# Optimization experiments

Measured on AMD Instinct MI355X. Metric: run time of the kernel, lower is better.

Reference implementation:

```python
import jax, jax.numpy as jnp
import numpy as np

NORM_EPS = 1e-8   # eps in F.normalize
PDIST_EPS = 1e-6  # eps in nn.PairwiseDistance(2, eps=1e-06): ||x1 - x2 + eps||_2


def setup_inputs() -> dict:
    key = jax.random.key(0)
    student_output = jax.random.normal(key, (16384, 1024), dtype=jnp.float32)
    return {"student_output": student_output}


def reference(student_output) -> jnp.ndarray:
    x = student_output
    n = x.shape[0]
    # --- pairwise NN via inner products on L2-normalized vectors (no-grad in original) ---
    norms = jnp.linalg.norm(x, axis=-1, keepdims=True)
    xn = x / jnp.maximum(norms, NORM_EPS)          # F.normalize(x, p=2, eps=1e-8)
    dots = xn @ xn.T                               # [N, N]
    dots = dots.at[jnp.diag_indices(n)].set(-1.0)  # mask self-similarity
    I = jnp.argmax(dots, axis=1)                   # nearest neighbor indices
    # --- pairwise L2 distance to NN (torch adds eps to the difference) ---
    diff = x - x[I] + PDIST_EPS                    # [N, D]
    distances = jnp.sqrt(jnp.sum(diff * diff, axis=-1))
    loss = -jnp.mean(jnp.log(distances))
    return loss
```

## Files before the change

### kernel.cpp

```cpp
#include <hip/hip_runtime.h>
#include <hip/hip_bf16.h>

#define KN 16384
#define KD 1024
#define NB (KN / 128)

typedef __attribute__((ext_vector_type(4))) int   i32x4;
typedef __attribute__((ext_vector_type(8))) int   i32x8;
typedef __attribute__((ext_vector_type(4))) float f32x4;

#define SCALE_M6 0x79797979
#define FMT_FP4  4

__device__ __forceinline__ i32x8 ldg_frag4(const unsigned char* p) {
  const i32x4 v = *(const i32x4*)p;
  return __builtin_shufflevector(v, v, 0, 1, 2, 3, -1, -1, -1, -1);
}

#define IDX_MASK 0x3FFFu
#define VAL_MASK 0xFFFFC000u

__device__ __forceinline__ unsigned fp4n(float x) {
  const float a = fabsf(x);
  unsigned c = (unsigned)(a >= 0.25f) + (unsigned)(a >= 0.75f)
             + (unsigned)(a >= 1.25f) + (unsigned)(a >= 1.75f)
             + (unsigned)(a >= 2.5f)  + (unsigned)(a >= 3.5f)
             + (unsigned)(a >= 5.0f);
  return c | ((__float_as_uint(x) >> 28) & 8u);
}
__device__ __forceinline__ unsigned short pack4(float4 v, float s) {
  return (unsigned short)(fp4n(v.x * s)        | (fp4n(v.y * s) << 4) |
                          (fp4n(v.z * s) << 8) | (fp4n(v.w * s) << 12));
}

__global__ __launch_bounds__(256) void k_normalize(const float* __restrict__ x,
                                                   unsigned char* __restrict__ xn,
                                                   unsigned* __restrict__ best) {
  const int lane = threadIdx.x & 63;
  const int wave = threadIdx.x >> 6;
  const int row  = (blockIdx.x << 2) + wave;
  if (lane == 0) best[row] = 0u;
  const float4* xr = (const float4*)(x + (size_t)row * KD);
  const float4 v0 = xr[lane];
  const float4 v1 = xr[lane + 64];
  const float4 v2 = xr[lane + 128];
  const float4 v3 = xr[lane + 192];
  float ss = v0.x * v0.x + v0.y * v0.y + v0.z * v0.z + v0.w * v0.w
           + v1.x * v1.x + v1.y * v1.y + v1.z * v1.z + v1.w * v1.w
           + v2.x * v2.x + v2.y * v2.y + v2.z * v2.z + v2.w * v2.w
           + v3.x * v3.x + v3.y * v3.y + v3.z * v3.z + v3.w * v3.w;
#pragma unroll
  for (int off = 32; off > 0; off >>= 1) ss += __shfl_xor(ss, off);
  const float scale = 64.0f / fmaxf(sqrtf(ss), 1e-8f);
  const unsigned short s0 = pack4(v0, scale);
  const unsigned short s1 = pack4(v1, scale);
  const unsigned short s2 = pack4(v2, scale);
  const unsigned short s3 = pack4(v3, scale);
  unsigned char* base = xn + ((size_t)(row >> 4) << 13) + (((lane >> 3) & 3) << 8)
                      + ((row & 15) << 4) + ((lane & 7) << 1) + ((lane >> 5) << 10);
  *(unsigned short*)(base)        = s0;
  *(unsigned short*)(base + 2048) = s1;
  *(unsigned short*)(base + 4096) = s2;
  *(unsigned short*)(base + 6144) = s3;
}

template <bool DIAG>
__device__ __forceinline__ void epilogue(const f32x4 (&acc)[4][4], int by, int bx,
                                         int wm, int wn, int quad, int l15,
                                         unsigned* __restrict__ best) {
  const int rowbase = (by << 7) + wm * 64 + (quad << 2);
  const int colbase = (bx << 7) + wn * 64 + l15;
  unsigned cm0 = 0u, cm1 = 0u, cm2 = 0u, cm3 = 0u;
#pragma unroll
  for (int i = 0; i < 4; i++) {
#pragma unroll
    for (int r = 0; r < 4; r++) {
      const int grow = rowbase + i * 16 + r;
      const unsigned grx = (unsigned)grow ^ IDX_MASK;
      unsigned rm = 0u;
#pragma unroll
      for (int j = 0; j < 4; j++) {
        const int gcol = colbase + j * 16;
        unsigned t = (__float_as_uint(fmaf(acc[i][j][r], 0.125f, 3.0f)) << 9) & VAL_MASK;
        if (DIAG && gcol == grow) t = 0u;
        const unsigned rc = t | ((unsigned)gcol ^ IDX_MASK);
        const unsigned cc = t | grx;
        rm = rm > rc ? rm : rc;
        if (j == 0) cm0 = cm0 > cc ? cm0 : cc;
        if (j == 1) cm1 = cm1 > cc ? cm1 : cc;
        if (j == 2) cm2 = cm2 > cc ? cm2 : cc;
        if (j == 3) cm3 = cm3 > cc ? cm3 : cc;
      }
#pragma unroll
      for (int off = 1; off < 16; off <<= 1) {
        const unsigned o = __shfl_xor(rm, off);
        rm = rm > o ? rm : o;
      }
      if (l15 == 0) atomicMax(best + grow, rm);
    }
  }
  if (!DIAG) {
    unsigned cm[4] = {cm0, cm1, cm2, cm3};
#pragma unroll
    for (int j = 0; j < 4; j++) {
      unsigned o = __shfl_xor(cm[j], 16);
      cm[j] = cm[j] > o ? cm[j] : o;
      o = __shfl_xor(cm[j], 32);
      cm[j] = cm[j] > o ? cm[j] : o;
      if (quad == 0) atomicMax(best + colbase + j * 16, cm[j]);
    }
  }
}

__global__ __launch_bounds__(256, 4) void k_nn_argmax(const unsigned char* __restrict__ xn,
                                                      unsigned* __restrict__ best) {
  const int id = blockIdx.x;
  int d, by;
  if (id < 8192) {
    const int o   = id & 7;
    const int idp = id >> 3;
    const int k   = idp >> 6;
    const int p   = idp & 63;
    const int q   = o + (k << 3);
    by = ((q & 15) << 3) + (p & 7);
    d  = ((q >> 4) << 3) + (p >> 3);
  } else {
    d  = NB / 2;
    by = id - 8192;
  }
  const int bx = (by + d) & (NB - 1);

  const int tid  = threadIdx.x;
  const int lane = tid & 63;
  const int wave = tid >> 6;
  const int wm   = wave >> 1;
  const int wn   = wave & 1;
  const int quad = lane >> 4;
  const int l15  = lane & 15;

  f32x4 acc[4][4];
#pragma unroll
  for (int i = 0; i < 4; i++)
#pragma unroll
    for (int j = 0; j < 4; j++) acc[i][j] = (f32x4){0.f, 0.f, 0.f, 0.f};

  const unsigned char* pa = xn + ((size_t)((by << 3) + (wm << 2)) << 13) + (lane << 4);
  const unsigned char* pb = xn + ((size_t)((bx << 3) + (wn << 2)) << 13) + (lane << 4);

#pragma unroll 2
  for (int kb = 0; kb < 8; kb++) {
    const int ko = kb << 10;
    const i32x8 a0 = ldg_frag4(pa + ko);
    const i32x8 a1 = ldg_frag4(pa + (1 << 13) + ko);
    const i32x8 a2 = ldg_frag4(pa + (2 << 13) + ko);
    const i32x8 a3 = ldg_frag4(pa + (3 << 13) + ko);
    const i32x8 b0 = ldg_frag4(pb + ko);
    const i32x8 b1 = ldg_frag4(pb + (1 << 13) + ko);
    const i32x8 b2 = ldg_frag4(pb + (2 << 13) + ko);
    const i32x8 b3 = ldg_frag4(pb + (3 << 13) + ko);
    acc[0][0] = __builtin_amdgcn_mfma_scale_f32_16x16x128_f8f6f4(a0, b0, acc[0][0], FMT_FP4, FMT_FP4, 0, SCALE_M6, 0, SCALE_M6);
    acc[1][0] = __builtin_amdgcn_mfma_scale_f32_16x16x128_f8f6f4(a1, b0, acc[1][0], FMT_FP4, FMT_FP4, 0, SCALE_M6, 0, SCALE_M6);
    acc[2][0] = __builtin_amdgcn_mfma_scale_f32_16x16x128_f8f6f4(a2, b0, acc[2][0], FMT_FP4, FMT_FP4, 0, SCALE_M6, 0, SCALE_M6);
    acc[3][0] = __builtin_amdgcn_mfma_scale_f32_16x16x128_f8f6f4(a3, b0, acc[3][0], FMT_FP4, FMT_FP4, 0, SCALE_M6, 0, SCALE_M6);
    acc[0][1] = __builtin_amdgcn_mfma_scale_f32_16x16x128_f8f6f4(a0, b1, acc[0][1], FMT_FP4, FMT_FP4, 0, SCALE_M6, 0, SCALE_M6);
    acc[1][1] = __builtin_amdgcn_mfma_scale_f32_16x16x128_f8f6f4(a1, b1, acc[1][1], FMT_FP4, FMT_FP4, 0, SCALE_M6, 0, SCALE_M6);
    acc[2][1] = __builtin_amdgcn_mfma_scale_f32_16x16x128_f8f6f4(a2, b1, acc[2][1], FMT_FP4, FMT_FP4, 0, SCALE_M6, 0, SCALE_M6);
    acc[3][1] = __builtin_amdgcn_mfma_scale_f32_16x16x128_f8f6f4(a3, b1, acc[3][1], FMT_FP4, FMT_FP4, 0, SCALE_M6, 0, SCALE_M6);
    acc[0][2] = __builtin_amdgcn_mfma_scale_f32_16x16x128_f8f6f4(a0, b2, acc[0][2], FMT_FP4, FMT_FP4, 0, SCALE_M6, 0, SCALE_M6);
    acc[1][2] = __builtin_amdgcn_mfma_scale_f32_16x16x128_f8f6f4(a1, b2, acc[1][2], FMT_FP4, FMT_FP4, 0, SCALE_M6, 0, SCALE_M6);
    acc[2][2] = __builtin_amdgcn_mfma_scale_f32_16x16x128_f8f6f4(a2, b2, acc[2][2], FMT_FP4, FMT_FP4, 0, SCALE_M6, 0, SCALE_M6);
    acc[3][2] = __builtin_amdgcn_mfma_scale_f32_16x16x128_f8f6f4(a3, b2, acc[3][2], FMT_FP4, FMT_FP4, 0, SCALE_M6, 0, SCALE_M6);
    acc[0][3] = __builtin_amdgcn_mfma_scale_f32_16x16x128_f8f6f4(a0, b3, acc[0][3], FMT_FP4, FMT_FP4, 0, SCALE_M6, 0, SCALE_M6);
    acc[1][3] = __builtin_amdgcn_mfma_scale_f32_16x16x128_f8f6f4(a1, b3, acc[1][3], FMT_FP4, FMT_FP4, 0, SCALE_M6, 0, SCALE_M6);
    acc[2][3] = __builtin_amdgcn_mfma_scale_f32_16x16x128_f8f6f4(a2, b3, acc[2][3], FMT_FP4, FMT_FP4, 0, SCALE_M6, 0, SCALE_M6);
    acc[3][3] = __builtin_amdgcn_mfma_scale_f32_16x16x128_f8f6f4(a3, b3, acc[3][3], FMT_FP4, FMT_FP4, 0, SCALE_M6, 0, SCALE_M6);
  }

  if (d == 0) epilogue<true>(acc, by, bx, wm, wn, quad, l15, best);
  else        epilogue<false>(acc, by, bx, wm, wn, quad, l15, best);
}

__global__ __launch_bounds__(256) void k_dist(const float* __restrict__ x,
                                              const unsigned* __restrict__ best,
                                              float* __restrict__ rowlog) {
  const int lane = threadIdx.x & 63;
  const int wave = threadIdx.x >> 6;
  const int row  = (blockIdx.x << 2) + wave;
  const int nb   = (int)((~best[row]) & IDX_MASK);
  const float4* ar = (const float4*)(x + (size_t)row * KD);
  const float4* br = (const float4*)(x + (size_t)nb * KD);
  float ss = 0.f;
#pragma unroll
  for (int q = 0; q < 4; q++) {
    const float4 a = ar[lane + 64 * q];
    const float4 b = br[lane + 64 * q];
    const float dx = a.x - b.x + 1e-6f;
    const float dy = a.y - b.y + 1e-6f;
    const float dz = a.z - b.z + 1e-6f;
    const float dw = a.w - b.w + 1e-6f;
    ss += dx * dx + dy * dy + dz * dz + dw * dw;
  }
#pragma unroll
  for (int off = 32; off > 0; off >>= 1) ss += __shfl_xor(ss, off);
  if (lane == 0) rowlog[row] = -logf(sqrtf(ss));
}

__global__ __launch_bounds__(1024) void k_final(const float* __restrict__ rowlog,
                                                float* __restrict__ out) {
  const int tid = threadIdx.x;
  float s = 0.f;
  for (int i = tid; i < KN; i += 1024) s += rowlog[i];
#pragma unroll
  for (int off = 32; off > 0; off >>= 1) s += __shfl_down(s, off);
  __shared__ float ws[16];
  if ((tid & 63) == 0) ws[tid >> 6] = s;
  __syncthreads();
  if (tid == 0) {
    float t = 0.f;
#pragma unroll
    for (int i = 0; i < 16; i++) t += ws[i];
    out[0] = t / (float)KN;
  }
}

extern "C" void kernel_launch(void* const* d_in, const int* in_sizes, int n_in,
                              void* d_out, int out_size, void* d_ws, size_t ws_size,
                              hipStream_t stream) {
  const float* x = (const float*)d_in[0];
  float* out = (float*)d_out;

  char* ws = (char*)d_ws;
  unsigned char* xn = (unsigned char*)ws;
  unsigned* best = (unsigned*)(ws + (size_t)KN * KD / 2);
  float* rowlog = (float*)(ws + (size_t)KN * KD / 2 + (size_t)KN * 4);

  k_normalize<<<KN / 4, 256, 0, stream>>>(x, xn, best);
  k_nn_argmax<<<8192 + 64, 256, 0, stream>>>(xn, best);
  k_dist<<<KN / 4, 256, 0, stream>>>(x, best, rowlog);
  k_final<<<1, 1024, 0, stream>>>(rowlog, out);
}
```

Baseline: 241.9 us.

## Stage FP4 tiles through double-buffered LDS with global_load_lds

Each wave used to load its A and B fragments straight from global memory, so every row chunk was fetched by two waves of the block. Now the four waves cooperatively copy the block's A and B K-slices into a double-buffered 32 KB shared-memory tile with direct global-to-LDS loads. The MFMA fragments are then read from LDS, and the next slice is prefetched while the current one is computed. This halves global/L2 fetches per block, but it adds a barrier per K step and LDS usage, and the min-blocks launch bound is relaxed, which may reduce occupancy.

```diff
diff --git a/kernel.cpp b/kernel.cpp
--- a/kernel.cpp
+++ b/kernel.cpp
@@ -9,10 +9,13 @@
 typedef __attribute__((ext_vector_type(8))) int   i32x8;
 typedef __attribute__((ext_vector_type(4))) float f32x4;
 
+typedef __attribute__((address_space(1))) unsigned int gu32;
+typedef __attribute__((address_space(3))) unsigned int su32;
+
 #define SCALE_M6 0x79797979
 #define FMT_FP4  4
 
-__device__ __forceinline__ i32x8 ldg_frag4(const unsigned char* p) {
+__device__ __forceinline__ i32x8 frag4(const unsigned char* p) {
   const i32x4 v = *(const i32x4*)p;
   return __builtin_shufflevector(v, v, 0, 1, 2, 3, -1, -1, -1, -1);
 }
@@ -112,8 +115,10 @@
   }
 }
 
-__global__ __launch_bounds__(256, 4) void k_nn_argmax(const unsigned char* __restrict__ xn,
-                                                      unsigned* __restrict__ best) {
+__global__ __launch_bounds__(256) void k_nn_argmax(const unsigned char* __restrict__ xn,
+                                                   unsigned* __restrict__ best) {
+  __shared__ unsigned char smem[2][16384];
+
   const int id = blockIdx.x;
   int d, by;
   if (id < 8192) {
@@ -144,20 +149,39 @@
 #pragma unroll
     for (int j = 0; j < 4; j++) acc[i][j] = (f32x4){0.f, 0.f, 0.f, 0.f};
 
-  const unsigned char* pa = xn + ((size_t)((by << 3) + (wm << 2)) << 13) + (lane << 4);
-  const unsigned char* pb = xn + ((size_t)((bx << 3) + (wn << 2)) << 13) + (lane << 4);
-
-#pragma unroll 2
+  const int c0 = wave << 2;
+  const int g0 = (wave & 2) ? ((bx << 3) + (c0 & 7)) : ((by << 3) + c0);
+  const unsigned char* sbase = xn + ((size_t)g0 << 13) + (lane << 4);
+
+  const int aoff = (wm << 12) + (lane << 4);
+  const int boff = 8192 + (wn << 12) + (lane << 4);
+
+#pragma unroll
+  for (int t = 0; t < 4; t++)
+    __builtin_amdgcn_global_load_lds((const gu32*)(const void*)(sbase + ((size_t)t << 13)),
+                                     (su32*)(void*)(&smem[0][(c0 + t) << 10]), 16, 0, 0);
+
+#pragma unroll
   for (int kb = 0; kb < 8; kb++) {
-    const int ko = kb << 10;
-    const i32x8 a0 = ldg_frag4(pa + ko);
-    const i32x8 a1 = ldg_frag4(pa + (1 << 13) + ko);
-    const i32x8 a2 = ldg_frag4(pa + (2 << 13) + ko);
-    const i32x8 a3 = ldg_frag4(pa + (3 << 13) + ko);
-    const i32x8 b0 = ldg_frag4(pb + ko);
-    const i32x8 b1 = ldg_frag4(pb + (1 << 13) + ko);
-    const i32x8 b2 = ldg_frag4(pb + (2 << 13) + ko);
-    const i32x8 b3 = ldg_frag4(pb + (3 << 13) + ko);
+    const int buf = kb & 1;
+    __syncthreads();
+    if (kb < 7) {
+#pragma unroll
+      for (int t = 0; t < 4; t++)
+        __builtin_amdgcn_global_load_lds(
+            (const gu32*)(const void*)(sbase + ((size_t)t << 13) + ((size_t)(kb + 1) << 10)),
+            (su32*)(void*)(&smem[buf ^ 1][(c0 + t) << 10]), 16, 0, 0);
+    }
+    const unsigned char* A = &smem[buf][aoff];
+    const unsigned char* B = &smem[buf][boff];
+    const i32x8 a0 = frag4(A);
+    const i32x8 a1 = frag4(A + 1024);
+    const i32x8 a2 = frag4(A + 2048);
+    const i32x8 a3 = frag4(A + 3072);
+    const i32x8 b0 = frag4(B);
+    const i32x8 b1 = frag4(B + 1024);
+    const i32x8 b2 = frag4(B + 2048);
+    const i32x8 b3 = frag4(B + 3072);
     acc[0][0] = __builtin_amdgcn_mfma_scale_f32_16x16x128_f8f6f4(a0, b0, acc[0][0], FMT_FP4, FMT_FP4, 0, SCALE_M6, 0, SCALE_M6);
     acc[1][0] = __builtin_amdgcn_mfma_scale_f32_16x16x128_f8f6f4(a1, b0, acc[1][0], FMT_FP4, FMT_FP4, 0, SCALE_M6, 0, SCALE_M6);
     acc[2][0] = __builtin_amdgcn_mfma_scale_f32_16x16x128_f8f6f4(a2, b0, acc[2][0], FMT_FP4, FMT_FP4, 0, SCALE_M6, 0, SCALE_M6);
```

After: 250.3 us. 1.03x slower.

## Stage A row panel in LDS and reuse it across eight diagonal tiles

Applied to the files above, without the earlier changes.

The argmax GEMM kernel now launches one block per row-block and diagonal group instead of one block per tile. Each block copies its 64KB FP4 A panel into shared memory with global_load_lds, then loops over 8 column tiles. Inside that loop, A fragments are read from LDS and only B still comes from global memory. This halves global/L2 fragment traffic and cuts block launch count. In exchange, 64KB of LDS per block limits occupancy, the 4-block launch bound is dropped, the panel load has no overlap with compute, and the d=64 tail now runs 128 blocks that compute mirrored duplicate tiles.

```diff
diff --git a/kernel.cpp b/kernel.cpp
--- a/kernel.cpp
+++ b/kernel.cpp
@@ -9,10 +9,13 @@
 typedef __attribute__((ext_vector_type(8))) int   i32x8;
 typedef __attribute__((ext_vector_type(4))) float f32x4;
 
+typedef __attribute__((address_space(1))) unsigned int gu32;
+typedef __attribute__((address_space(3))) unsigned int su32;
+
 #define SCALE_M6 0x79797979
 #define FMT_FP4  4
 
-__device__ __forceinline__ i32x8 ldg_frag4(const unsigned char* p) {
+__device__ __forceinline__ i32x8 frag4(const unsigned char* p) {
   const i32x4 v = *(const i32x4*)p;
   return __builtin_shufflevector(v, v, 0, 1, 2, 3, -1, -1, -1, -1);
 }
@@ -112,23 +115,14 @@
   }
 }
 
-__global__ __launch_bounds__(256, 4) void k_nn_argmax(const unsigned char* __restrict__ xn,
-                                                      unsigned* __restrict__ best) {
+__global__ __launch_bounds__(256) void k_nn_argmax(const unsigned char* __restrict__ xn,
+                                                   unsigned* __restrict__ best) {
+  __shared__ unsigned char As[65536];
+
   const int id = blockIdx.x;
-  int d, by;
-  if (id < 8192) {
-    const int o   = id & 7;
-    const int idp = id >> 3;
-    const int k   = idp >> 6;
-    const int p   = idp & 63;
-    const int q   = o + (k << 3);
-    by = ((q & 15) << 3) + (p & 7);
-    d  = ((q >> 4) << 3) + (p >> 3);
-  } else {
-    d  = NB / 2;
-    by = id - 8192;
-  }
-  const int bx = (by + d) & (NB - 1);
+  int by, d0, ntiles;
+  if (id < 1024) { by = id & 127; d0 = (id >> 7) << 3; ntiles = 8; }
+  else           { by = id - 1024; d0 = 64;            ntiles = 1; }
 
   const int tid  = threadIdx.x;
   const int lane = tid & 63;
@@ -138,46 +132,60 @@
   const int quad = lane >> 4;
   const int l15  = lane & 15;
 
-  f32x4 acc[4][4];
-#pragma unroll
-  for (int i = 0; i < 4; i++)
-#pragma unroll
-    for (int j = 0; j < 4; j++) acc[i][j] = (f32x4){0.f, 0.f, 0.f, 0.f};
-
-  const unsigned char* pa = xn + ((size_t)((by << 3) + (wm << 2)) << 13) + (lane << 4);
-  const unsigned char* pb = xn + ((size_t)((bx << 3) + (wn << 2)) << 13) + (lane << 4);
+  const unsigned char* srcA = xn + ((size_t)(by << 6) << 10) + (lane << 4);
+#pragma unroll
+  for (int t = 0; t < 16; t++) {
+    const int c = (wave << 4) + t;
+    __builtin_amdgcn_global_load_lds((const gu32*)(const void*)(srcA + ((size_t)c << 10)),
+                                     (su32*)(void*)(&As[c << 10]), 16, 0, 0);
+  }
+  __syncthreads();
+
+  const int aoff = (wm << 15) + (lane << 4);
+
+  for (int t = 0; t < ntiles; t++) {
+    const int d  = d0 + t;
+    const int bx = (by + d) & (NB - 1);
+    const unsigned char* pb = xn + ((size_t)((bx << 3) + (wn << 2)) << 13) + (lane << 4);
+
+    f32x4 acc[4][4];
+#pragma unroll
+    for (int i = 0; i < 4; i++)
+#pragma unroll
+      for (int j = 0; j < 4; j++) acc[i][j] = (f32x4){0.f, 0.f, 0.f, 0.f};
 
 #pragma unroll 2
-  for (int kb = 0; kb < 8; kb++) {
-    const int ko = kb << 10;
-    const i32x8 a0 = ldg_frag4(pa + ko);
-    const i32x8 a1 = ldg_frag4(pa + (1 << 13) + ko);
-    const i32x8 a2 = ldg_frag4(pa + (2 << 13) + ko);
-    const i32x8 a3 = ldg_frag4(pa + (3 << 13) + ko);
-    const i32x8 b0 = ldg_frag4(pb + ko);
-    const i32x8 b1 = ldg_frag4(pb + (1 << 13) + ko);
-    const i32x8 b2 = ldg_frag4(pb + (2 << 13) + ko);
-    const i32x8 b3 = ldg_frag4(pb + (3 << 13) + ko);
-    acc[0][0] = __builtin_amdgcn_mfma_scale_f32_16x16x128_f8f6f4(a0, b0, acc[0][0], FMT_FP4, FMT_FP4, 0, SCALE_M6, 0, SCALE_M6);
-    acc[1][0] = __builtin_amdgcn_mfma_scale_f32_16x16x128_f8f6f4(a1, b0, acc[1][0], FMT_FP4, FMT_FP4, 0, SCALE_M6, 0, SCALE_M6);
-    acc[2][0] = __builtin_amdgcn_mfma_scale_f32_16x16x128_f8f6f4(a2, b0, acc[2][0], FMT_FP4, FMT_FP4, 0, SCALE_M6, 0, SCALE_M6);
-    acc[3][0] = __builtin_amdgcn_mfma_scale_f32_16x16x128_f8f6f4(a3, b0, acc[3][0], FMT_FP4, FMT_FP4, 0, SCALE_M6, 0, SCALE_M6);
-    acc[0][1] = __builtin_amdgcn_mfma_scale_f32_16x16x128_f8f6f4(a0, b1, acc[0][1], FMT_FP4, FMT_FP4, 0, SCALE_M6, 0, SCALE_M6);
-    acc[1][1] = __builtin_amdgcn_mfma_scale_f32_16x16x128_f8f6f4(a1, b1, acc[1][1], FMT_FP4, FMT_FP4, 0, SCALE_M6, 0, SCALE_M6);
-    acc[2][1] = __builtin_amdgcn_mfma_scale_f32_16x16x128_f8f6f4(a2, b1, acc[2][1], FMT_FP4, FMT_FP4, 0, SCALE_M6, 0, SCALE_M6);
-    acc[3][1] = __builtin_amdgcn_mfma_scale_f32_16x16x128_f8f6f4(a3, b1, acc[3][1], FMT_FP4, FMT_FP4, 0, SCALE_M6, 0, SCALE_M6);
-    acc[0][2] = __builtin_amdgcn_mfma_scale_f32_16x16x128_f8f6f4(a0, b2, acc[0][2], FMT_FP4, FMT_FP4, 0, SCALE_M6, 0, SCALE_M6);
-    acc[1][2] = __builtin_amdgcn_mfma_scale_f32_16x16x128_f8f6f4(a1, b2, acc[1][2], FMT_FP4, FMT_FP4, 0, SCALE_M6, 0, SCALE_M6);
-    acc[2][2] = __builtin_amdgcn_mfma_scale_f32_16x16x128_f8f6f4(a2, b2, acc[2][2], FMT_FP4, FMT_FP4, 0, SCALE_M6, 0, SCALE_M6);
-    acc[3][2] = __builtin_amdgcn_mfma_scale_f32_16x16x128_f8f6f4(a3, b2, acc[3][2], FMT_FP4, FMT_FP4, 0, SCALE_M6, 0, SCALE_M6);
-    acc[0][3] = __builtin_amdgcn_mfma_scale_f32_16x16x128_f8f6f4(a0, b3, acc[0][3], FMT_FP4, FMT_FP4, 0, SCALE_M6, 0, SCALE_M6);
-    acc[1][3] = __builtin_amdgcn_mfma_scale_f32_16x16x128_f8f6f4(a1, b3, acc[1][3], FMT_FP4, FMT_FP4, 0, SCALE_M6, 0, SCALE_M6);
-    acc[2][3] = __builtin_amdgcn_mfma_scale_f32_16x16x128_f8f6f4(a2, b3, acc[2][3], FMT_FP4, FMT_FP4, 0, SCALE_M6, 0, SCALE_M6);
-    acc[3][3] = __builtin_amdgcn_mfma_scale_f32_16x16x128_f8f6f4(a3, b3, acc[3][3], FMT_FP4, FMT_FP4, 0, SCALE_M6, 0, SCALE_M6);
-  }
-
-  if (d == 0) epilogue<true>(acc, by, bx, wm, wn, quad, l15, best);
-  else        epilogue<false>(acc, by, bx, wm, wn, quad, l15, best);
+    for (int kb = 0; kb < 8; kb++) {
+      const int ko = kb << 10;
+      const i32x8 a0 = frag4(&As[aoff + ko]);
+      const i32x8 a1 = frag4(&As[aoff + 8192 + ko]);
+      const i32x8 a2 = frag4(&As[aoff + 16384 + ko]);
+      const i32x8 a3 = frag4(&As[aoff + 24576 + ko]);
+      const i32x8 b0 = frag4(pb + ko);
+      const i32x8 b1 = frag4(pb + 8192 + ko);
+      const i32x8 b2 = frag4(pb + 16384 + ko);
+      const i32x8 b3 = frag4(pb + 24576 + ko);
+      acc[0][0] = __builtin_amdgcn_mfma_scale_f32_16x16x128_f8f6f4(a0, b0, acc[0][0], FMT_FP4, FMT_FP4, 0, SCALE_M6, 0, SCALE_M6);
+      acc[1][0] = __builtin_amdgcn_mfma_scale_f32_16x16x128_f8f6f4(a1, b0, acc[1][0], FMT_FP4, FMT_FP4, 0, SCALE_M6, 0, SCALE_M6);
+      acc[2][0] = __builtin_amdgcn_mfma_scale_f32_16x16x128_f8f6f4(a2, b0, acc[2][0], FMT_FP4, FMT_FP4, 0, SCALE_M6, 0, SCALE_M6);
+      acc[3][0] = __builtin_amdgcn_mfma_scale_f32_16x16x128_f8f6f4(a3, b0, acc[3][0], FMT_FP4, FMT_FP4, 0, SCALE_M6, 0, SCALE_M6);
+      acc[0][1] = __builtin_amdgcn_mfma_scale_f32_16x16x128_f8f6f4(a0, b1, acc[0][1], FMT_FP4, FMT_FP4, 0, SCALE_M6, 0, SCALE_M6);
+      acc[1][1] = __builtin_amdgcn_mfma_scale_f32_16x16x128_f8f6f4(a1, b1, acc[1][1], FMT_FP4, FMT_FP4, 0, SCALE_M6, 0, SCALE_M6);
+      acc[2][1] = __builtin_amdgcn_mfma_scale_f32_16x16x128_f8f6f4(a2, b1, acc[2][1], FMT_FP4, FMT_FP4, 0, SCALE_M6, 0, SCALE_M6);
+      acc[3][1] = __builtin_amdgcn_mfma_scale_f32_16x16x128_f8f6f4(a3, b1, acc[3][1], FMT_FP4, FMT_FP4, 0, SCALE_M6, 0, SCALE_M6);
+      acc[0][2] = __builtin_amdgcn_mfma_scale_f32_16x16x128_f8f6f4(a0, b2, acc[0][2], FMT_FP4, FMT_FP4, 0, SCALE_M6, 0, SCALE_M6);
+      acc[1][2] = __builtin_amdgcn_mfma_scale_f32_16x16x128_f8f6f4(a1, b2, acc[1][2], FMT_FP4, FMT_FP4, 0, SCALE_M6, 0, SCALE_M6);
+      acc[2][2] = __builtin_amdgcn_mfma_scale_f32_16x16x128_f8f6f4(a2, b2, acc[2][2], FMT_FP4, FMT_FP4, 0, SCALE_M6, 0, SCALE_M6);
+      acc[3][2] = __builtin_amdgcn_mfma_scale_f32_16x16x128_f8f6f4(a3, b2, acc[3][2], FMT_FP4, FMT_FP4, 0, SCALE_M6, 0, SCALE_M6);
+      acc[0][3] = __builtin_amdgcn_mfma_scale_f32_16x16x128_f8f6f4(a0, b3, acc[0][3], FMT_FP4, FMT_FP4, 0, SCALE_M6, 0, SCALE_M6);
+      acc[1][3] = __builtin_amdgcn_mfma_scale_f32_16x16x128_f8f6f4(a1, b3, acc[1][3], FMT_FP4, FMT_FP4, 0, SCALE_M6, 0, SCALE_M6);
+      acc[2][3] = __builtin_amdgcn_mfma_scale_f32_16x16x128_f8f6f4(a2, b3, acc[2][3], FMT_FP4, FMT_FP4, 0, SCALE_M6, 0, SCALE_M6);
+      acc[3][3] = __builtin_amdgcn_mfma_scale_f32_16x16x128_f8f6f4(a3, b3, acc[3][3], FMT_FP4, FMT_FP4, 0, SCALE_M6, 0, SCALE_M6);
+    }
+
+    if (d == 0) epilogue<true>(acc, by, bx, wm, wn, quad, l15, best);
+    else        epilogue<false>(acc, by, bx, wm, wn, quad, l15, best);
+  }
 }
 
 __global__ __launch_bounds__(256) void k_dist(const float* __restrict__ x,
@@ -235,7 +243,7 @@
   float* rowlog = (float*)(ws + (size_t)KN * KD / 2 + (size_t)KN * 4);
 
   k_normalize<<<KN / 4, 256, 0, stream>>>(x, xn, best);
-  k_nn_argmax<<<8192 + 64, 256, 0, stream>>>(xn, best);
+  k_nn_argmax<<<1024 + 128, 256, 0, stream>>>(xn, best);
   k_dist<<<KN / 4, 256, 0, stream>>>(x, best, rowlog);
   k_final<<<1, 1024, 0, stream>>>(rowlog, out);
 }
```

Result: slower. 363.1 us (+50.1%).
